# Kernel tuning notes

Measured on AMD Instinct MI355X. Metric: run time of the kernel, lower is better.

The kernel has to match this reference:

```python
import jax, jax.numpy as jnp
import numpy as np

EMBED_DIM = 1024
BATCH, SEQ = 4, 2048


def setup_inputs() -> dict:
    key = jax.random.key(0)
    k1, k2 = jax.random.split(key)
    hidden_states = jax.random.normal(k1, (BATCH, SEQ, EMBED_DIM), dtype=jnp.float32)
    # fused QKV projection weight (Linear(embed_dim, 3*embed_dim, bias=False)),
    # stored as [E, 3E] so y = x @ W
    W_qkv = jax.random.normal(k2, (EMBED_DIM, 3 * EMBED_DIM), dtype=jnp.float32) * (1.0 / np.sqrt(EMBED_DIM))
    return {"hidden_states": hidden_states, "W_qkv": W_qkv}


def reference(hidden_states, W_qkv):
    E = hidden_states.shape[-1]
    scale = 1.0 / np.sqrt(E)
    qkv = jnp.einsum('bse,ef->bsf', hidden_states, W_qkv)  # [B,S,3E]
    q, k, v = jnp.split(qkv, 3, axis=-1)                   # each [B,S,E]
    # scores = q @ (k^T * scale); softmax over keys
    scores = jnp.einsum('bqe,bke->bqk', q, k) * scale      # [B,S,S]
    w = jax.nn.softmax(scores, axis=-1)
    return jnp.einsum('bqk,bke->bqe', w, v)                # [B,S,E]
```

## Files before the change

kernel.cpp:

```cpp
#include <hip/hip_runtime.h>

typedef __attribute__((ext_vector_type(8))) short short8;
typedef __attribute__((ext_vector_type(8))) unsigned short ushort8;
typedef __attribute__((ext_vector_type(4))) float f32x4;

__device__ __forceinline__ float bf2f(unsigned short u) {
  union { unsigned int u; float f; } c; c.u = ((unsigned int)u) << 16; return c.f;
}
__device__ __forceinline__ unsigned short f2bf(float f) {
  union { float f; unsigned int u; } c; c.f = f;
  unsigned int x = c.u;
  return (unsigned short)((x + 0x7FFFu + ((x >> 16) & 1u)) >> 16);
}

#define GLD_LDS16(g, l)                                                        \
  __builtin_amdgcn_global_load_lds(                                            \
      (const __attribute__((address_space(1))) void*)(g),                      \
      (__attribute__((address_space(3))) void*)(l), 16, 0, 0)

__global__ __launch_bounds__(256) void prep_kernel(
    const float* __restrict__ X, unsigned short* __restrict__ Xb,
    const float* __restrict__ W, unsigned short* __restrict__ Wt) {
  const int t = threadIdx.x;
  if (blockIdx.x < 4096) {
    long i = ((long)blockIdx.x * 256 + t) * 8;
    float4 a = *(const float4*)(X + i);
    float4 b = *(const float4*)(X + i + 4);
    ushort8 o;
    o[0] = f2bf(a.x); o[1] = f2bf(a.y); o[2] = f2bf(a.z); o[3] = f2bf(a.w);
    o[4] = f2bf(b.x); o[5] = f2bf(b.y); o[6] = f2bf(b.z); o[7] = f2bf(b.w);
    *(ushort8*)(Xb + i) = o;
  } else {
    const int bid = blockIdx.x - 4096;
    const int f0 = (bid % 48) * 64;
    const int e0 = (bid / 48) * 64;
    __shared__ unsigned short tile[64][65];
    const int cg = (t & 15) * 4;
    const int r = t >> 4;
#pragma unroll
    for (int i = 0; i < 4; ++i) {
      int e = r + i * 16;
      float4 v = *(const float4*)(W + (long)(e0 + e) * 3072 + f0 + cg);
      tile[e][cg + 0] = f2bf(v.x);
      tile[e][cg + 1] = f2bf(v.y);
      tile[e][cg + 2] = f2bf(v.z);
      tile[e][cg + 3] = f2bf(v.w);
    }
    __syncthreads();
#pragma unroll
    for (int i = 0; i < 4; ++i) {
      int f = (t >> 4) + i * 16;
      int e = (t & 15) * 4;
      ushort4 o;
      o.x = tile[e + 0][f];
      o.y = tile[e + 1][f];
      o.z = tile[e + 2][f];
      o.w = tile[e + 3][f];
      *(ushort4*)(Wt + (long)(f0 + f) * 1024 + e0 + e) = o;
    }
  }
}

__global__ __launch_bounds__(256) void transpose_v_kernel(
    const unsigned short* __restrict__ QKV, unsigned short* __restrict__ Vt) {
  const int s0 = blockIdx.x * 64;
  const int e0 = blockIdx.y * 64;
  const int b = blockIdx.z;
  const unsigned short* V = QKV + (long)b * 2048 * 3072 + 2048;
  unsigned short* VtB = Vt + (long)b * 1024 * 2048;
  __shared__ unsigned short tile[64][65];
  const int t = threadIdx.x;
#pragma unroll
  for (int i = 0; i < 2; ++i) {
    int s = (t >> 3) + i * 32;
    int e = (t & 7) * 8;
    ushort8 v = *(const ushort8*)(V + (long)(s0 + s) * 3072 + e0 + e);
#pragma unroll
    for (int k = 0; k < 8; ++k) tile[s][e + k] = v[k];
  }
  __syncthreads();
#pragma unroll
  for (int i = 0; i < 2; ++i) {
    int e = (t >> 3) + i * 32;
    int s = (t & 7) * 8;
    ushort8 o;
#pragma unroll
    for (int k = 0; k < 8; ++k) o[k] = tile[s + k][e];
    *(ushort8*)(VtB + (long)(e0 + e) * 2048 + s0 + s) = o;
  }
}

template <bool BF16OUT>
__global__ __launch_bounds__(256, 2) void gemm_bt_kernel(
    const unsigned short* __restrict__ A, const unsigned short* __restrict__ B,
    void* __restrict__ Cv, int K, int lda, int ldb, int ldc,
    long sA, long sB, long sC, float alpha) {
  constexpr int BM = 128, BN = 128, BK = 64;
  __shared__ __align__(16) unsigned short As[BM * BK];
  __shared__ __align__(16) unsigned short Bs[BN * BK];

  const int t = threadIdx.x;
  const int lane = t & 63;
  const int wave = t >> 6;
  const int quad = lane >> 4;
  const int mrow = lane & 15;
  const int wm = wave >> 1, wn = wave & 1;

  const int rowA0 = blockIdx.y * BM;
  const int rowB0 = blockIdx.x * BN;
  const int b = blockIdx.z;
  const unsigned short* Ab = A + (long)b * sA;
  const unsigned short* Bb = B + (long)b * sB;

  f32x4 acc[4][4];
#pragma unroll
  for (int i = 0; i < 4; ++i)
#pragma unroll
    for (int j = 0; j < 4; ++j) {
      f32x4 z = {0.f, 0.f, 0.f, 0.f};
      acc[i][j] = z;
    }

  const int rbase = wave * 32 + (lane >> 3);
  const int c2 = lane & 7;

  for (int kt = 0; kt < K; kt += BK) {
#pragma unroll
    for (int j = 0; j < 4; ++j) {
      int r = rbase + j * 8;
      int c = c2 ^ (r & 7);
      GLD_LDS16(Ab + (long)(rowA0 + r) * lda + kt + c * 8, As + (wave * 4 + j) * 512);
      GLD_LDS16(Bb + (long)(rowB0 + r) * ldb + kt + c * 8, Bs + (wave * 4 + j) * 512);
    }
    __syncthreads();
#pragma unroll
    for (int ks = 0; ks < 2; ++ks) {
      short8 af[4], bfr[4];
#pragma unroll
      for (int i = 0; i < 4; ++i) {
        int rA = wm * 64 + i * 16 + mrow;
        int cc = ks * 4 + quad;
        af[i] = *(const short8*)(As + (rA * 8 + (cc ^ (rA & 7))) * 8);
        int rB = wn * 64 + i * 16 + mrow;
        bfr[i] = *(const short8*)(Bs + (rB * 8 + (cc ^ (rB & 7))) * 8);
      }
#pragma unroll
      for (int mt = 0; mt < 4; ++mt)
#pragma unroll
        for (int nt = 0; nt < 4; ++nt)
          acc[mt][nt] = __builtin_amdgcn_mfma_f32_16x16x32_bf16(
              af[mt], bfr[nt], acc[mt][nt], 0, 0, 0);
    }
    __syncthreads();
  }

  const int m_base = rowA0 + wm * 64;
  const int n_base = rowB0 + wn * 64;
  const long cb = (long)b * sC;
#pragma unroll
  for (int mt = 0; mt < 4; ++mt)
#pragma unroll
    for (int nt = 0; nt < 4; ++nt)
#pragma unroll
      for (int i = 0; i < 4; ++i) {
        int row = m_base + mt * 16 + quad * 4 + i;
        int col = n_base + nt * 16 + mrow;
        float v = acc[mt][nt][i] * alpha;
        if constexpr (BF16OUT) {
          ((unsigned short*)Cv)[cb + (long)row * ldc + col] = f2bf(v);
        } else {
          ((float*)Cv)[cb + (long)row * ldc + col] = v;
        }
      }
}

__global__ __launch_bounds__(256) void softmax_kernel(unsigned short* __restrict__ S) {
  const int row = blockIdx.x;
  const int t = threadIdx.x;
  const int lane = t & 63, wave = t >> 6;
  unsigned short* rp = S + (long)row * 2048 + t * 8;
  ushort8 v = *(const ushort8*)rp;
  float x[8];
#pragma unroll
  for (int k = 0; k < 8; ++k) x[k] = bf2f(v[k]);
  float m = x[0];
#pragma unroll
  for (int k = 1; k < 8; ++k) m = fmaxf(m, x[k]);
#pragma unroll
  for (int off = 32; off > 0; off >>= 1) m = fmaxf(m, __shfl_xor(m, off, 64));
  __shared__ float red[8];
  if (lane == 0) red[wave] = m;
  __syncthreads();
  m = fmaxf(fmaxf(red[0], red[1]), fmaxf(red[2], red[3]));
  float e[8];
  float s = 0.f;
#pragma unroll
  for (int k = 0; k < 8; ++k) {
    e[k] = __expf(x[k] - m);
    s += e[k];
  }
#pragma unroll
  for (int off = 32; off > 0; off >>= 1) s += __shfl_xor(s, off, 64);
  if (lane == 0) red[4 + wave] = s;
  __syncthreads();
  float L = red[4] + red[5] + red[6] + red[7];
  float inv = 1.0f / L;
  ushort8 o;
#pragma unroll
  for (int k = 0; k < 8; ++k) o[k] = f2bf(e[k] * inv);
  *(ushort8*)rp = o;
}

extern "C" void kernel_launch(void* const* d_in, const int* in_sizes, int n_in,
                              void* d_out, int out_size, void* d_ws, size_t ws_size,
                              hipStream_t stream) {
  const float* X = (const float*)d_in[0];
  const float* W = (const float*)d_in[1];
  float* out = (float*)d_out;

  char* ws = (char*)d_ws;
  unsigned short* Xb  = (unsigned short*)(ws);
  unsigned short* Wtb = (unsigned short*)(ws + 16777216);
  unsigned short* QKV = (unsigned short*)(ws + 23068672);
  unsigned short* Vt  = (unsigned short*)(ws + 73400320);
  unsigned short* Sb  = (unsigned short*)(ws + 90177536);

  prep_kernel<<<4864, 256, 0, stream>>>(X, Xb, W, Wtb);

  gemm_bt_kernel<true><<<dim3(24, 64, 1), 256, 0, stream>>>(
      Xb, Wtb, QKV, 1024, 1024, 1024, 3072, 0L, 0L, 0L, 1.0f);

  transpose_v_kernel<<<dim3(32, 16, 4), 256, 0, stream>>>(QKV, Vt);

  gemm_bt_kernel<true><<<dim3(16, 16, 4), 256, 0, stream>>>(
      QKV, QKV + 1024, Sb, 1024, 3072, 3072, 2048,
      (long)2048 * 3072, (long)2048 * 3072, (long)2048 * 2048, 0.03125f);

  softmax_kernel<<<8192, 256, 0, stream>>>(Sb);

  gemm_bt_kernel<false><<<dim3(8, 16, 4), 256, 0, stream>>>(
      Sb, Vt, out, 2048, 2048, 2048, 1024,
      (long)2048 * 2048, (long)1024 * 2048, (long)2048 * 1024, 1.0f);
}
```

Baseline: 250.5 us.

## Prefetch next GEMM K-tile into registers while computing current tile

```diff
diff --git a/kernel.cpp b/kernel.cpp
--- a/kernel.cpp
+++ b/kernel.cpp
@@ -12,11 +12,6 @@
   unsigned int x = c.u;
   return (unsigned short)((x + 0x7FFFu + ((x >> 16) & 1u)) >> 16);
 }
-
-#define GLD_LDS16(g, l)                                                        \
-  __builtin_amdgcn_global_load_lds(                                            \
-      (const __attribute__((address_space(1))) void*)(g),                      \
-      (__attribute__((address_space(3))) void*)(l), 16, 0, 0)
 
 __global__ __launch_bounds__(256) void prep_kernel(
     const float* __restrict__ X, unsigned short* __restrict__ Xb,
@@ -124,15 +119,32 @@
   const int rbase = wave * 32 + (lane >> 3);
   const int c2 = lane & 7;
 
-  for (int kt = 0; kt < K; kt += BK) {
-#pragma unroll
-    for (int j = 0; j < 4; ++j) {
-      int r = rbase + j * 8;
-      int c = c2 ^ (r & 7);
-      GLD_LDS16(Ab + (long)(rowA0 + r) * lda + kt + c * 8, As + (wave * 4 + j) * 512);
-      GLD_LDS16(Bb + (long)(rowB0 + r) * ldb + kt + c * 8, Bs + (wave * 4 + j) * 512);
-    }
-    __syncthreads();
+  float4 stg_a[4], stg_b[4];
+#pragma unroll
+  for (int j = 0; j < 4; ++j) {
+    int r = rbase + j * 8;
+    int c = c2 ^ (r & 7);
+    stg_a[j] = *(const float4*)(Ab + (long)(rowA0 + r) * lda + c * 8);
+    stg_b[j] = *(const float4*)(Bb + (long)(rowB0 + r) * ldb + c * 8);
+  }
+#pragma unroll
+  for (int j = 0; j < 4; ++j) {
+    *(float4*)(As + (wave * 4 + j) * 512 + lane * 8) = stg_a[j];
+    *(float4*)(Bs + (wave * 4 + j) * 512 + lane * 8) = stg_b[j];
+  }
+  __syncthreads();
+
+  for (int kt = BK; kt < K + BK; kt += BK) {
+    const bool more = kt < K;
+    if (more) {
+#pragma unroll
+      for (int j = 0; j < 4; ++j) {
+        int r = rbase + j * 8;
+        int c = c2 ^ (r & 7);
+        stg_a[j] = *(const float4*)(Ab + (long)(rowA0 + r) * lda + kt + c * 8);
+        stg_b[j] = *(const float4*)(Bb + (long)(rowB0 + r) * ldb + kt + c * 8);
+      }
+    }
 #pragma unroll
     for (int ks = 0; ks < 2; ++ks) {
       short8 af[4], bfr[4];
@@ -151,7 +163,15 @@
           acc[mt][nt] = __builtin_amdgcn_mfma_f32_16x16x32_bf16(
               af[mt], bfr[nt], acc[mt][nt], 0, 0, 0);
     }
-    __syncthreads();
+    if (more) {
+      __syncthreads();
+#pragma unroll
+      for (int j = 0; j < 4; ++j) {
+        *(float4*)(As + (wave * 4 + j) * 512 + lane * 8) = stg_a[j];
+        *(float4*)(Bs + (wave * 4 + j) * 512 + lane * 8) = stg_b[j];
+      }
+      __syncthreads();
+    }
   }
 
   const int m_base = rowA0 + wm * 64;
```

Result: slower. 714.7 us (+185.3%).
